# Performance work log

Measured on AMD Instinct MI355X. Metric: run time of the kernel, lower is better.

## Reference

```python
import jax, jax.numpy as jnp
import numpy as np

N_NODES = 100000
N_EDGES = 3200000


def setup_inputs() -> dict:
    key = jax.random.key(0)
    ks = jax.random.split(key, 16)
    inp = {
        "noisy_coords": jax.random.normal(ks[0], (N_NODES, 3), dtype=jnp.float32),
        "atom_types": jax.random.randint(ks[1], (N_NODES,), 0, 2),
        "edge_index": jax.random.randint(ks[2], (2, N_EDGES), 0, N_NODES),
        "emb": jax.random.normal(ks[3], (2, 3), dtype=jnp.float32),
    }
    # GCNConv weights: 6->32->64->64->32->3 (hidden_dim=64)
    dims = [(6, 32), (32, 64), (64, 64), (64, 32), (32, 3)]
    for i, (din, dout) in enumerate(dims, start=1):
        inp[f"W{i}"] = jax.random.normal(ks[3 + i], (din, dout), dtype=jnp.float32) / np.sqrt(din).astype(np.float32)
        inp[f"b{i}"] = jnp.zeros((dout,), dtype=jnp.float32)
    return inp


def _gcn_conv(x, W, b, src, dst, norm, n):
    # GCNConv: X @ W, then symmetric-normalized scatter-add over edges, then bias.
    h = x @ W                       # [N, dout]
    msg = h[src] * norm[:, None]    # gather + edge normalization  [E+N, dout]
    return jax.ops.segment_sum(msg, dst, num_segments=n) + b


def reference(noisy_coords, atom_types, edge_index, emb,
              W1, b1, W2, b2, W3, b3, W4, b4, W5, b5):
    n = noisy_coords.shape[0]
    loop = jnp.arange(n)
    # PyG GCNConv adds self loops and uses deg^{-1/2} (A+I) deg^{-1/2} normalization
    src = jnp.concatenate([edge_index[0], loop])
    dst = jnp.concatenate([edge_index[1], loop])
    deg = jax.ops.segment_sum(jnp.ones(src.shape[0], dtype=jnp.float32), dst, num_segments=n)
    dinv = jnp.where(deg > 0, jax.lax.rsqrt(deg), 0.0)
    norm = dinv[src] * dinv[dst]    # [E+N]

    x = jnp.concatenate([noisy_coords, emb[atom_types]], axis=1)  # [N, 6]
    x = jax.nn.relu(_gcn_conv(x, W1, b1, src, dst, norm, n))
    x = jax.nn.relu(_gcn_conv(x, W2, b2, src, dst, norm, n))
    x = jax.nn.relu(_gcn_conv(x, W3, b3, src, dst, norm, n))
    x = jax.nn.relu(_gcn_conv(x, W4, b4, src, dst, norm, n))
    x = _gcn_conv(x, W5, b5, src, dst, norm, n)  # final layer: no relu
    return x
```

## Files before the change

### kernel.cpp

```cpp
#include <hip/hip_runtime.h>
#include <hip/hip_fp16.h>

#define NBLK_BIN 256
#define NBKT 196
#define BWIN 512
#define CAP 128


typedef unsigned int uint;

union U32H2 { uint u; __half2 h; };

__device__ inline float2 h2_to_f2(uint u) {
    U32H2 c; c.u = u;
    return __half22float2(c.h);
}
__device__ inline uint f2_to_h2(float a, float b) {
    U32H2 c; c.h = __floats2half2_rn(a, b);
    return c.u;
}

__global__ __launch_bounds__(1024) void bin_kernel(const int* __restrict__ src,
                                                   const int* __restrict__ dst,
                                                   int2* __restrict__ pairs,
                                                   int* __restrict__ blkcnt, int e) {
    __shared__ int lcnt[NBKT];
    int blk = blockIdx.x, tid = threadIdx.x;
    for (int t = tid; t < NBKT; t += 1024) lcnt[t] = 0;
    __syncthreads();
    int chunk = (e + NBLK_BIN - 1) / NBLK_BIN;
    int base = blk * chunk;
    int end = min(e, base + chunk);
    for (int i = base + tid; i < end; i += 1024) {
        int s = src[i], d = dst[i];
        int b = d >> 9;
        int pos = atomicAdd(&lcnt[b], 1);
        if (pos < CAP) pairs[((size_t)blk * NBKT + b) * CAP + pos] = make_int2(s, d);
    }
    __syncthreads();
    for (int t = tid; t < NBKT; t += 1024) blkcnt[blk * NBKT + t] = min(lcnt[t], CAP);
}

__global__ __launch_bounds__(1024) void fill_kernel(const int2* __restrict__ pairs,
                                                    const int* __restrict__ blkcnt,
                                                    int* __restrict__ srcs,
                                                    int* __restrict__ cnt,
                                                    int* __restrict__ rowptr,
                                                    float* __restrict__ dinv, int n) {
    __shared__ int lc[BWIN];
    __shared__ int ps[BWIN];
    __shared__ int sm[NBLK_BIN];
    __shared__ int gbase_s;
    int b = blockIdx.x, tid = threadIdx.x;
    int nbase = b << 9;
    if (tid < BWIN) lc[tid] = 0;
    for (int t = tid; t < NBLK_BIN; t += 1024) sm[t] = blkcnt[t * NBKT + b];
    if (tid == 0) gbase_s = 0;
    __syncthreads();
    {
        long long tot = (long long)NBLK_BIN * b;
        int lsum = 0;
        for (long long j = tid; j < tot; j += 1024) {
            int blk = (int)(j / b);
            int bp  = (int)(j - (long long)blk * b);
            lsum += blkcnt[blk * NBKT + bp];
        }
        for (int o = 32; o > 0; o >>= 1) lsum += __shfl_down(lsum, o, 64);
        if ((tid & 63) == 0 && lsum != 0) atomicAdd(&gbase_s, lsum);
    }
    int wave = tid >> 6, lane = tid & 63;
    for (int blk = wave; blk < NBLK_BIN; blk += 16) {
        int m = sm[blk];
        const int2* p = pairs + ((size_t)blk * NBKT + b) * CAP;
        for (int i = lane; i < m; i += 64) atomicAdd(&lc[p[i].y - nbase], 1);
    }
    __syncthreads();
    int myc = (tid < BWIN) ? lc[tid] : 0;
    if (tid < BWIN) ps[tid] = myc;
    __syncthreads();
    for (int off = 1; off < BWIN; off <<= 1) {
        int t = 0;
        if (tid < BWIN && tid >= off) t = ps[tid - off];
        __syncthreads();
        if (tid < BWIN) ps[tid] += t;
        __syncthreads();
    }
    int gbase = gbase_s;
    if (tid < BWIN) {
        int ex = ps[tid] - myc;
        int vtx = nbase + tid;
        if (vtx < n) {
            cnt[vtx] = myc;
            rowptr[vtx] = gbase + ex;
            dinv[vtx] = rsqrtf(1.0f + (float)myc);
        }
    }
    __syncthreads();
    if (tid < BWIN) lc[tid] = ps[tid] - myc;
    __syncthreads();
    for (int blk = wave; blk < NBLK_BIN; blk += 16) {
        int m = sm[blk];
        const int2* p = pairs + ((size_t)blk * NBKT + b) * CAP;
        for (int i = lane; i < m; i += 64) {
            int2 e2 = p[i];
            int o = atomicAdd(&lc[e2.y - nbase], 1);
            srcs[gbase + o] = e2.x;
        }
    }
}


__global__ __launch_bounds__(256) void build_x0_h_kernel(const float* __restrict__ coords,
                                                         const int* __restrict__ at,
                                                         const float* __restrict__ emb,
                                                         const float* __restrict__ dinv,
                                                         uint* __restrict__ x, int n) {
    int v = blockIdx.x * 256 + threadIdx.x;
    if (v >= n) return;
    float dv = dinv[v];
    float c0 = coords[3 * v + 0] * dv;
    float c1 = coords[3 * v + 1] * dv;
    float c2 = coords[3 * v + 2] * dv;
    int t = at[v];
    float e0 = emb[3 * t + 0] * dv;
    float e1 = emb[3 * t + 1] * dv;
    float e2 = emb[3 * t + 2] * dv;
    uint* row = x + (size_t)v * 4;
    row[0] = f2_to_h2(c0, c1);
    row[1] = f2_to_h2(c2, e0);
    row[2] = f2_to_h2(e1, e2);
    row[3] = 0;
}

template <int FPH2, bool HAS_BIAS, bool RELU>
__global__ __launch_bounds__(256) void agg_h_kernel(const uint* __restrict__ in,
                                                    const float* __restrict__ dinv,
                                                    const int* __restrict__ rowptr,
                                                    const int* __restrict__ cnt,
                                                    const int* __restrict__ srcs,
                                                    const float* __restrict__ bias,
                                                    uint* __restrict__ out, int n) {
    int gid = blockIdx.x * 256 + threadIdx.x;
    int v = gid / FPH2, j2 = gid % FPH2;
    if (v >= n) return;
    float2 s0 = h2_to_f2(in[(size_t)v * FPH2 + j2]);
    float accx = s0.x, accy = s0.y;
    int start = rowptr[v];
    int len = cnt[v];
    int k = 0;
    for (; k + 4 <= len; k += 4) {
        int sA = srcs[start + k];
        int sB = srcs[start + k + 1];
        int sC = srcs[start + k + 2];
        int sD = srcs[start + k + 3];
        float2 fA = h2_to_f2(in[(size_t)sA * FPH2 + j2]);
        float2 fB = h2_to_f2(in[(size_t)sB * FPH2 + j2]);
        float2 fC = h2_to_f2(in[(size_t)sC * FPH2 + j2]);
        float2 fD = h2_to_f2(in[(size_t)sD * FPH2 + j2]);
        accx += (fA.x + fB.x) + (fC.x + fD.x);
        accy += (fA.y + fB.y) + (fC.y + fD.y);
    }
    for (; k < len; ++k) {
        int s = srcs[start + k];
        float2 f = h2_to_f2(in[(size_t)s * FPH2 + j2]);
        accx += f.x; accy += f.y;
    }
    float dv = dinv[v];
    accx *= dv; accy *= dv;
    if (HAS_BIAS) { accx += bias[2 * j2]; accy += bias[2 * j2 + 1]; }
    if (RELU) { accx = fmaxf(accx, 0.0f); accy = fmaxf(accy, 0.0f); }
    out[(size_t)v * FPH2 + j2] = f2_to_h2(accx, accy);
}

template <int DIN, int DOUT, int DOUTH2, bool HAS_BIAS, bool RELU, bool SCALE, bool OUTF>
__global__ __launch_bounds__(256) void gemm_h_kernel(const uint* __restrict__ xin,
                                                     const float* __restrict__ W,
                                                     const float* __restrict__ bias,
                                                     const float* __restrict__ dinv,
                                                     void* __restrict__ xout,
                                                     int istride_u, int ostride, int n) {
    __shared__ float wlds[DIN * DOUT];
    for (int i = threadIdx.x; i < DIN * DOUT; i += 256) wlds[i] = W[i];
    __syncthreads();
    int gid = blockIdx.x * 256 + threadIdx.x;
    int v = gid / DOUTH2, j2 = gid % DOUTH2;
    if (v >= n) return;
    int j1 = 2 * j2;
    const uint* xr = xin + (size_t)v * istride_u;
    float acc0 = 0.0f, acc1 = 0.0f;
#pragma unroll
    for (int ku = 0; ku < DIN / 2; ++ku) {
        float2 xf = h2_to_f2(xr[ku]);
        int k = 2 * ku;
        acc0 = fmaf(xf.x, wlds[k * DOUT + j1], acc0);
        acc0 = fmaf(xf.y, wlds[(k + 1) * DOUT + j1], acc0);
        if (j1 + 1 < DOUT) {
            acc1 = fmaf(xf.x, wlds[k * DOUT + j1 + 1], acc1);
            acc1 = fmaf(xf.y, wlds[(k + 1) * DOUT + j1 + 1], acc1);
        }
    }
    if (HAS_BIAS) {
        acc0 += bias[j1];
        if (j1 + 1 < DOUT) acc1 += bias[j1 + 1];
    }
    if (RELU) { acc0 = fmaxf(acc0, 0.0f); acc1 = fmaxf(acc1, 0.0f); }
    if (SCALE) { float dv = dinv[v]; acc0 *= dv; acc1 *= dv; }
    if (OUTF) {
        float* o = (float*)xout + (size_t)v * ostride;
        o[j1] = acc0;
        if (j1 + 1 < DOUT) o[j1 + 1] = acc1;
    } else {
        ((uint*)xout)[(size_t)v * ostride + j2] = f2_to_h2(acc0, acc1);
    }
}

template <int F, int FP, bool HAS_BIAS, bool RELU>
__global__ __launch_bounds__(256) void agg_f_kernel(const float* __restrict__ in,
                                                    const float* __restrict__ dinv,
                                                    const int* __restrict__ rowptr,
                                                    const int* __restrict__ cnt,
                                                    const int* __restrict__ srcs,
                                                    const float* __restrict__ b,
                                                    float* __restrict__ out,
                                                    int istride, int ostride, int n) {
    int gid = blockIdx.x * 256 + threadIdx.x;
    int v = gid / FP, j = gid % FP;
    if (v >= n || j >= F) return;
    float dv = dinv[v];
    int start = rowptr[v];
    int len = cnt[v];
    float acc = in[(size_t)v * istride + j];
    int k = 0;
    for (; k + 4 <= len; k += 4) {
        int s0 = srcs[start + k];
        int s1 = srcs[start + k + 1];
        int s2 = srcs[start + k + 2];
        int s3 = srcs[start + k + 3];
        float a0 = in[(size_t)s0 * istride + j];
        float a1 = in[(size_t)s1 * istride + j];
        float a2 = in[(size_t)s2 * istride + j];
        float a3 = in[(size_t)s3 * istride + j];
        acc += (a0 + a1) + (a2 + a3);
    }
    for (; k < len; ++k) acc += in[(size_t)srcs[start + k] * istride + j];
    float val = acc * dv;
    if (HAS_BIAS) val += b[j];
    if (RELU) val = fmaxf(val, 0.0f);
    out[(size_t)v * ostride + j] = val;
}


extern "C" void kernel_launch(void* const* d_in, const int* in_sizes, int n_in,
                              void* d_out, int out_size, void* d_ws, size_t ws_size,
                              hipStream_t stream) {
    const float* coords = (const float*)d_in[0];
    const int* at       = (const int*)d_in[1];
    const int* ei       = (const int*)d_in[2];
    const float* emb    = (const float*)d_in[3];
    const float* W1 = (const float*)d_in[4];  const float* b1 = (const float*)d_in[5];
    const float* W2 = (const float*)d_in[6];  const float* b2 = (const float*)d_in[7];
    const float* W3 = (const float*)d_in[8];  const float* b3 = (const float*)d_in[9];
    const float* W4 = (const float*)d_in[10]; const float* b4 = (const float*)d_in[11];
    const float* W5 = (const float*)d_in[12]; const float* b5 = (const float*)d_in[13];
    float* out = (float*)d_out;

    const int n = in_sizes[0] / 3;
    const int e = in_sizes[2] / 2;
    const int* src = ei;
    const int* dst = ei + e;

    char* ws = (char*)d_ws;
    size_t off = 0;
    float* dinv   = (float*)(ws + off); off += (size_t)n * 4;
    int*   cnt    = (int*)(ws + off);   off += (size_t)n * 4;
    int*   rowptr = (int*)(ws + off);   off += (size_t)n * 4;
    int*   blkcnt = (int*)(ws + off);   off += (size_t)NBLK_BIN * NBKT * 4;
    int*   srcs   = (int*)(ws + off);   off += (size_t)e * 4;
    char*  alias  = ws + off;
    int2*  pairs  = (int2*)alias;
    uint*  A_h    = (uint*)alias;
    uint*  B_h    = A_h + (size_t)n * 32;
    float* B_f    = (float*)(B_h + (size_t)n * 32);

    int nb = (n + 255) / 256;

    bin_kernel<<<NBLK_BIN, 1024, 0, stream>>>(src, dst, pairs, blkcnt, e);
    fill_kernel<<<NBKT, 1024, 0, stream>>>(pairs, blkcnt, srcs, cnt, rowptr, dinv, n);

    build_x0_h_kernel<<<nb, 256, 0, stream>>>(coords, at, emb, dinv, A_h, n);

    auto blocks = [](long long threads) { return (int)((threads + 255) / 256); };

    agg_h_kernel<4, false, false><<<blocks((long long)n * 4), 256, 0, stream>>>(
        A_h, dinv, rowptr, cnt, srcs, nullptr, B_h, n);
    gemm_h_kernel<6, 32, 16, true, true, true, false><<<blocks((long long)n * 16), 256, 0, stream>>>(
        B_h, W1, b1, dinv, A_h, 4, 16, n);

    agg_h_kernel<16, false, false><<<blocks((long long)n * 16), 256, 0, stream>>>(
        A_h, dinv, rowptr, cnt, srcs, nullptr, B_h, n);
    gemm_h_kernel<32, 64, 32, true, true, true, false><<<blocks((long long)n * 32), 256, 0, stream>>>(
        B_h, W2, b2, dinv, A_h, 16, 32, n);

    agg_h_kernel<32, false, false><<<blocks((long long)n * 32), 256, 0, stream>>>(
        A_h, dinv, rowptr, cnt, srcs, nullptr, B_h, n);
    gemm_h_kernel<64, 64, 32, true, true, false, false><<<blocks((long long)n * 32), 256, 0, stream>>>(
        B_h, W3, b3, dinv, A_h, 32, 32, n);

    gemm_h_kernel<64, 32, 16, false, false, true, false><<<blocks((long long)n * 16), 256, 0, stream>>>(
        A_h, W4, nullptr, dinv, B_h, 32, 16, n);
    agg_h_kernel<16, true, true><<<blocks((long long)n * 16), 256, 0, stream>>>(
        B_h, dinv, rowptr, cnt, srcs, b4, A_h, n);

    gemm_h_kernel<32, 3, 2, false, false, true, true><<<blocks((long long)n * 2), 256, 0, stream>>>(
        A_h, W5, nullptr, dinv, B_f, 16, 4, n);
    agg_f_kernel<3, 4, true, false><<<blocks((long long)n * 4), 256, 0, stream>>>(
        B_f, dinv, rowptr, cnt, srcs, b5, out, 4, 3, n);
}
```

Measured before the change: 452.6 us.

## Fuse layer-3/4 GEMMs and fold layer-5 GEMM into layer-4 aggregation

Layer 3's and layer 4's dense transforms now run in one kernel. The 64-wide intermediate stays in LDS, so it no longer round-trips through global memory. The layer-5 32->3 projection moves into the layer-4 aggregation epilogue and uses a 16-lane shuffle reduction, so the separate GEMM launch and its fp16 store/reload disappear. The cost is a larger LDS footprint per block, which can lower occupancy, plus extra shuffle work in the aggregation kernel.

After: 430.7 us. -4.8%, faster.

```diff
diff --git a/kernel.cpp b/kernel.cpp
--- a/kernel.cpp
+++ b/kernel.cpp
@@ -172,12 +172,65 @@
     out[(size_t)v * FPH2 + j2] = f2_to_h2(accx, accy);
 }
 
-template <int DIN, int DOUT, int DOUTH2, bool HAS_BIAS, bool RELU, bool SCALE, bool OUTF>
+__global__ __launch_bounds__(256) void agg_l4l5_kernel(const uint* __restrict__ in,
+                                                       const float* __restrict__ dinv,
+                                                       const int* __restrict__ rowptr,
+                                                       const int* __restrict__ cnt,
+                                                       const int* __restrict__ srcs,
+                                                       const float* __restrict__ b4,
+                                                       const float* __restrict__ W5,
+                                                       float* __restrict__ outf, int n) {
+    int gid = blockIdx.x * 256 + threadIdx.x;
+    int v = gid / 16, j2 = gid % 16;
+    if (v >= n) return;
+    float2 s0 = h2_to_f2(in[(size_t)v * 16 + j2]);
+    float accx = s0.x, accy = s0.y;
+    int start = rowptr[v];
+    int len = cnt[v];
+    int k = 0;
+    for (; k + 4 <= len; k += 4) {
+        int sA = srcs[start + k];
+        int sB = srcs[start + k + 1];
+        int sC = srcs[start + k + 2];
+        int sD = srcs[start + k + 3];
+        float2 fA = h2_to_f2(in[(size_t)sA * 16 + j2]);
+        float2 fB = h2_to_f2(in[(size_t)sB * 16 + j2]);
+        float2 fC = h2_to_f2(in[(size_t)sC * 16 + j2]);
+        float2 fD = h2_to_f2(in[(size_t)sD * 16 + j2]);
+        accx += (fA.x + fB.x) + (fC.x + fD.x);
+        accy += (fA.y + fB.y) + (fC.y + fD.y);
+    }
+    for (; k < len; ++k) {
+        int s = srcs[start + k];
+        float2 f = h2_to_f2(in[(size_t)s * 16 + j2]);
+        accx += f.x; accy += f.y;
+    }
+    float dv = dinv[v];
+    accx *= dv; accy *= dv;
+    accx += b4[2 * j2]; accy += b4[2 * j2 + 1];
+    accx = fmaxf(accx, 0.0f); accy = fmaxf(accy, 0.0f);
+    int j1 = 2 * j2;
+    float p0 = accx * W5[j1 * 3 + 0] + accy * W5[(j1 + 1) * 3 + 0];
+    float p1 = accx * W5[j1 * 3 + 1] + accy * W5[(j1 + 1) * 3 + 1];
+    float p2 = accx * W5[j1 * 3 + 2] + accy * W5[(j1 + 1) * 3 + 2];
+#pragma unroll
+    for (int m = 1; m < 16; m <<= 1) {
+        p0 += __shfl_xor(p0, m, 16);
+        p1 += __shfl_xor(p1, m, 16);
+        p2 += __shfl_xor(p2, m, 16);
+    }
+    if (j2 < 3) {
+        float o = (j2 == 0) ? p0 : (j2 == 1 ? p1 : p2);
+        outf[(size_t)v * 4 + j2] = o * dv;
+    }
+}
+
+template <int DIN, int DOUT, int DOUTH2, bool HAS_BIAS, bool RELU, bool SCALE>
 __global__ __launch_bounds__(256) void gemm_h_kernel(const uint* __restrict__ xin,
                                                      const float* __restrict__ W,
                                                      const float* __restrict__ bias,
                                                      const float* __restrict__ dinv,
-                                                     void* __restrict__ xout,
+                                                     uint* __restrict__ xout,
                                                      int istride_u, int ostride, int n) {
     __shared__ float wlds[DIN * DOUT];
     for (int i = threadIdx.x; i < DIN * DOUT; i += 256) wlds[i] = W[i];
@@ -205,12 +258,60 @@
     }
     if (RELU) { acc0 = fmaxf(acc0, 0.0f); acc1 = fmaxf(acc1, 0.0f); }
     if (SCALE) { float dv = dinv[v]; acc0 *= dv; acc1 *= dv; }
-    if (OUTF) {
-        float* o = (float*)xout + (size_t)v * ostride;
-        o[j1] = acc0;
-        if (j1 + 1 < DOUT) o[j1 + 1] = acc1;
-    } else {
-        ((uint*)xout)[(size_t)v * ostride + j2] = f2_to_h2(acc0, acc1);
+    xout[(size_t)v * ostride + j2] = f2_to_h2(acc0, acc1);
+}
+
+#define G34_NODES 16
+__global__ __launch_bounds__(256) void gemm34_kernel(const uint* __restrict__ xin,
+                                                     const float* __restrict__ W3,
+                                                     const float* __restrict__ b3,
+                                                     const float* __restrict__ W4,
+                                                     const float* __restrict__ dinv,
+                                                     uint* __restrict__ xout,
+                                                     int n) {
+    __shared__ float w3[64 * 64];
+    __shared__ float w4[64 * 32];
+    __shared__ float hb[G34_NODES][65];
+    for (int i = threadIdx.x; i < 64 * 64; i += 256) w3[i] = W3[i];
+    for (int i = threadIdx.x; i < 64 * 32; i += 256) w4[i] = W4[i];
+    __syncthreads();
+    int i  = threadIdx.x >> 4;
+    int j2 = threadIdx.x & 15;
+    int v  = blockIdx.x * G34_NODES + i;
+    bool ok = (v < n);
+    int j1 = 2 * j2;
+    float a0 = 0.f, a1 = 0.f, a2 = 0.f, a3 = 0.f;
+    if (ok) {
+        const uint* xr = xin + (size_t)v * 32;
+#pragma unroll
+        for (int ku = 0; ku < 32; ++ku) {
+            float2 xf = h2_to_f2(xr[ku]);
+            int k = 2 * ku;
+            a0 = fmaf(xf.x, w3[k * 64 + j1],      a0);
+            a0 = fmaf(xf.y, w3[(k + 1) * 64 + j1],      a0);
+            a1 = fmaf(xf.x, w3[k * 64 + j1 + 1],  a1);
+            a1 = fmaf(xf.y, w3[(k + 1) * 64 + j1 + 1],  a1);
+            a2 = fmaf(xf.x, w3[k * 64 + j1 + 32], a2);
+            a2 = fmaf(xf.y, w3[(k + 1) * 64 + j1 + 32], a2);
+            a3 = fmaf(xf.x, w3[k * 64 + j1 + 33], a3);
+            a3 = fmaf(xf.y, w3[(k + 1) * 64 + j1 + 33], a3);
+        }
+        hb[i][j1]      = fmaxf(a0 + b3[j1],      0.f);
+        hb[i][j1 + 1]  = fmaxf(a1 + b3[j1 + 1],  0.f);
+        hb[i][j1 + 32] = fmaxf(a2 + b3[j1 + 32], 0.f);
+        hb[i][j1 + 33] = fmaxf(a3 + b3[j1 + 33], 0.f);
+    }
+    __syncthreads();
+    float c0 = 0.f, c1 = 0.f;
+#pragma unroll
+    for (int k = 0; k < 64; ++k) {
+        float hk = hb[i][k];
+        c0 = fmaf(hk, w4[k * 32 + j1],     c0);
+        c1 = fmaf(hk, w4[k * 32 + j1 + 1], c1);
+    }
+    if (ok) {
+        float dv = dinv[v];
+        xout[(size_t)v * 16 + j2] = f2_to_h2(c0 * dv, c1 * dv);
     }
 }
 
@@ -293,26 +394,22 @@
 
     agg_h_kernel<4, false, false><<<blocks((long long)n * 4), 256, 0, stream>>>(
         A_h, dinv, rowptr, cnt, srcs, nullptr, B_h, n);
-    gemm_h_kernel<6, 32, 16, true, true, true, false><<<blocks((long long)n * 16), 256, 0, stream>>>(
+    gemm_h_kernel<6, 32, 16, true, true, true><<<blocks((long long)n * 16), 256, 0, stream>>>(
         B_h, W1, b1, dinv, A_h, 4, 16, n);
 
     agg_h_kernel<16, false, false><<<blocks((long long)n * 16), 256, 0, stream>>>(
         A_h, dinv, rowptr, cnt, srcs, nullptr, B_h, n);
-    gemm_h_kernel<32, 64, 32, true, true, true, false><<<blocks((long long)n * 32), 256, 0, stream>>>(
+    gemm_h_kernel<32, 64, 32, true, true, true><<<blocks((long long)n * 32), 256, 0, stream>>>(
         B_h, W2, b2, dinv, A_h, 16, 32, n);
 
     agg_h_kernel<32, false, false><<<blocks((long long)n * 32), 256, 0, stream>>>(
         A_h, dinv, rowptr, cnt, srcs, nullptr, B_h, n);
-    gemm_h_kernel<64, 64, 32, true, true, false, false><<<blocks((long long)n * 32), 256, 0, stream>>>(
-        B_h, W3, b3, dinv, A_h, 32, 32, n);
-
-    gemm_h_kernel<64, 32, 16, false, false, true, false><<<blocks((long long)n * 16), 256, 0, stream>>>(
-        A_h, W4, nullptr, dinv, B_h, 32, 16, n);
-    agg_h_kernel<16, true, true><<<blocks((long long)n * 16), 256, 0, stream>>>(
-        B_h, dinv, rowptr, cnt, srcs, b4, A_h, n);
-
-    gemm_h_kernel<32, 3, 2, false, false, true, true><<<blocks((long long)n * 2), 256, 0, stream>>>(
-        A_h, W5, nullptr, dinv, B_f, 16, 4, n);
+    gemm34_kernel<<<(n + G34_NODES - 1) / G34_NODES, 256, 0, stream>>>(
+        B_h, W3, b3, W4, dinv, A_h, n);
+
+    agg_l4l5_kernel<<<blocks((long long)n * 16), 256, 0, stream>>>(
+        A_h, dinv, rowptr, cnt, srcs, b4, W5, B_f, n);
+
     agg_f_kernel<3, 4, true, false><<<blocks((long long)n * 4), 256, 0, stream>>>(
         B_f, dinv, rowptr, cnt, srcs, b5, out, 4, 3, n);
 }
```
